# Optimization experiments

Hardware: AMD Instinct MI355X
Metric: run time of the kernel (lower is better)

## Reference

```python
import jax, jax.numpy as jnp
import numpy as np
import math

INPUT_SIZE = 2048
OUTPUT_SIZE = 10000
EPS = 1e-8


def _hadamard_cropped(rows, cols):
    # Sylvester Hadamard: H[i, j] = (-1) ** popcount(i & j), built only on the
    i = np.arange(rows, dtype=np.int64)[:, None]
    j = np.arange(cols, dtype=np.int64)[None, :]
    a = i & j
    nbits = max(rows, cols).bit_length()
    parity = np.zeros((rows, cols), dtype=np.int64)
    for k in range(nbits):
        parity += (a >> k) & 1
    return (1 - 2 * (parity & 1)).astype(np.float32)


def setup_inputs() -> dict:
    key = jax.random.key(0)
    kx, kb = jax.random.split(key)
    init_scale = 1.0 / math.sqrt(OUTPUT_SIZE)
    x = jax.random.normal(kx, (16384, INPUT_SIZE), dtype=jnp.float32)
    proj = jnp.asarray(_hadamard_cropped(OUTPUT_SIZE, INPUT_SIZE))
    scale = jnp.full((1,), init_scale, dtype=jnp.float32)
    bias = jax.random.uniform(kb, (OUTPUT_SIZE,), dtype=jnp.float32,
                              minval=-init_scale, maxval=init_scale)
    return {"x": x, "proj": proj, "scale": scale, "bias": bias}


def reference(x, proj, scale, bias):
    # L2-normalize along last dim (norm + eps, matching torch semantics)
    xn = x / (jnp.linalg.norm(x, axis=-1, keepdims=True) + EPS)
    # linear with cropped Hadamard matrix: [B, in] @ [out, in]^T -> [B, out]
    out = -scale * jnp.einsum('bi,oi->bo', xn, proj)
    return out + bias[None, :]
```

## Files before the change

kernel.cpp:

```cpp
#include <hip/hip_runtime.h>
#include <math.h>


constexpr int N_IN  = 2048;
constexpr int N_OUT = 10000;
constexpr int ROWS_PER_BLOCK = 4;

__global__ __launch_bounds__(256, 5) void fwht_proj_kernel(
    const float* __restrict__ x,
    const float* __restrict__ scale,
    const float* __restrict__ bias,
    float* __restrict__ out)
{
    __shared__ float lds[ROWS_PER_BLOCK * N_IN];

    const int wave = threadIdx.x >> 6;
    const int lane = threadIdx.x & 63;
    const int row  = (blockIdx.x << 2) + wave;

    const float* __restrict__ xrow = x + (size_t)row * N_IN;

    float v[32];
    float ss = 0.0f;
#pragma unroll
    for (int j = 0; j < 32; ++j) {
        v[j] = xrow[j * 64 + lane];
        ss = fmaf(v[j], v[j], ss);
    }
#pragma unroll
    for (int m = 1; m < 64; m <<= 1)
        ss += __shfl_xor(ss, m, 64);
    const float inv = 1.0f / (sqrtf(ss) + 1e-8f);

#pragma unroll
    for (int m = 1; m <= 32; m <<= 1) {
        const bool lo = (lane & m) == 0;
#pragma unroll
        for (int j = 0; j < 32; ++j) {
            float o = __shfl_xor(v[j], m, 64);
            v[j] = lo ? (v[j] + o) : (o - v[j]);
        }
    }
#pragma unroll
    for (int jm = 1; jm <= 16; jm <<= 1) {
#pragma unroll
        for (int j = 0; j < 32; ++j) {
            if ((j & jm) == 0) {
                const float a = v[j], b = v[j ^ jm];
                v[j]      = a + b;
                v[j ^ jm] = a - b;
            }
        }
    }

    float* __restrict__ my = lds + wave * N_IN;
#pragma unroll
    for (int j = 0; j < 32; ++j)
        my[j * 64 + lane] = v[j];

    __syncthreads();

    const float s = -scale[0] * inv;
    float* __restrict__ orow = out + (size_t)row * N_OUT;

    for (int idx = lane; idx < N_OUT / 4; idx += 64) {
        const int o = idx << 2;
        const float4 y  = *reinterpret_cast<const float4*>(my + (o & (N_IN - 1)));
        const float4 bv = *reinterpret_cast<const float4*>(bias + o);
        float4 r;
        r.x = fmaf(s, y.x, bv.x);
        r.y = fmaf(s, y.y, bv.y);
        r.z = fmaf(s, y.z, bv.z);
        r.w = fmaf(s, y.w, bv.w);
        *reinterpret_cast<float4*>(orow + o) = r;
    }
}

extern "C" void kernel_launch(void* const* d_in, const int* in_sizes, int n_in,
                              void* d_out, int out_size, void* d_ws, size_t ws_size,
                              hipStream_t stream) {
    const float* x     = (const float*)d_in[0];
    const float* scale = (const float*)d_in[2];
    const float* bias  = (const float*)d_in[3];
    float* out = (float*)d_out;

    const int rows = in_sizes[0] / N_IN;
    dim3 grid(rows / ROWS_PER_BLOCK), block(256);
    hipLaunchKernelGGL(fwht_proj_kernel, grid, block, 0, stream,
                       x, scale, bias, out);
}
```

Baseline: 165.1 us.

## Keep FWHT result in registers with float4 layout, drop LDS staging

```diff
diff --git a/kernel.cpp b/kernel.cpp
--- a/kernel.cpp
+++ b/kernel.cpp
@@ -1,31 +1,34 @@
 #include <hip/hip_runtime.h>
 #include <math.h>
 
+
+typedef float f32x4 __attribute__((ext_vector_type(4)));
 
 constexpr int N_IN  = 2048;
 constexpr int N_OUT = 10000;
 constexpr int ROWS_PER_BLOCK = 4;
 
-__global__ __launch_bounds__(256, 5) void fwht_proj_kernel(
+__global__ __launch_bounds__(256, 4) void fwht_proj_kernel(
     const float* __restrict__ x,
     const float* __restrict__ scale,
     const float* __restrict__ bias,
     float* __restrict__ out)
 {
-    __shared__ float lds[ROWS_PER_BLOCK * N_IN];
-
     const int wave = threadIdx.x >> 6;
     const int lane = threadIdx.x & 63;
     const int row  = (blockIdx.x << 2) + wave;
 
     const float* __restrict__ xrow = x + (size_t)row * N_IN;
 
-    float v[32];
+    f32x4 v[8];
     float ss = 0.0f;
 #pragma unroll
-    for (int j = 0; j < 32; ++j) {
-        v[j] = xrow[j * 64 + lane];
-        ss = fmaf(v[j], v[j], ss);
+    for (int j = 0; j < 8; ++j) {
+        v[j] = *reinterpret_cast<const f32x4*>(xrow + (j << 8) + (lane << 2));
+        ss = fmaf(v[j].x, v[j].x, ss);
+        ss = fmaf(v[j].y, v[j].y, ss);
+        ss = fmaf(v[j].z, v[j].z, ss);
+        ss = fmaf(v[j].w, v[j].w, ss);
     }
 #pragma unroll
     for (int m = 1; m < 64; m <<= 1)
@@ -33,46 +36,78 @@
     const float inv = 1.0f / (sqrtf(ss) + 1e-8f);
 
 #pragma unroll
+    for (int j = 0; j < 8; ++j) {
+        const f32x4 a = v[j];
+        f32x4 t;
+        t.x = a.x + a.y;  t.y = a.x - a.y;
+        t.z = a.z + a.w;  t.w = a.z - a.w;
+        f32x4 u;
+        u.x = t.x + t.z;  u.y = t.y + t.w;
+        u.z = t.x - t.z;  u.w = t.y - t.w;
+        v[j] = u;
+    }
+#pragma unroll
     for (int m = 1; m <= 32; m <<= 1) {
         const bool lo = (lane & m) == 0;
 #pragma unroll
-        for (int j = 0; j < 32; ++j) {
-            float o = __shfl_xor(v[j], m, 64);
+        for (int j = 0; j < 8; ++j) {
+            f32x4 o;
+            o.x = __shfl_xor(v[j].x, m, 64);
+            o.y = __shfl_xor(v[j].y, m, 64);
+            o.z = __shfl_xor(v[j].z, m, 64);
+            o.w = __shfl_xor(v[j].w, m, 64);
             v[j] = lo ? (v[j] + o) : (o - v[j]);
         }
     }
 #pragma unroll
-    for (int jm = 1; jm <= 16; jm <<= 1) {
+    for (int jm = 1; jm <= 4; jm <<= 1) {
 #pragma unroll
-        for (int j = 0; j < 32; ++j) {
+        for (int j = 0; j < 8; ++j) {
             if ((j & jm) == 0) {
-                const float a = v[j], b = v[j ^ jm];
+                const f32x4 a = v[j], b = v[j ^ jm];
                 v[j]      = a + b;
                 v[j ^ jm] = a - b;
             }
         }
     }
 
-    float* __restrict__ my = lds + wave * N_IN;
-#pragma unroll
-    for (int j = 0; j < 32; ++j)
-        my[j * 64 + lane] = v[j];
-
-    __syncthreads();
-
     const float s = -scale[0] * inv;
     float* __restrict__ orow = out + (size_t)row * N_OUT;
 
-    for (int idx = lane; idx < N_OUT / 4; idx += 64) {
-        const int o = idx << 2;
-        const float4 y  = *reinterpret_cast<const float4*>(my + (o & (N_IN - 1)));
-        const float4 bv = *reinterpret_cast<const float4*>(bias + o);
-        float4 r;
-        r.x = fmaf(s, y.x, bv.x);
-        r.y = fmaf(s, y.y, bv.y);
-        r.z = fmaf(s, y.z, bv.z);
-        r.w = fmaf(s, y.w, bv.w);
-        *reinterpret_cast<float4*>(orow + o) = r;
+#pragma unroll
+    for (int w = 0; w < 4; ++w) {
+#pragma unroll 4
+        for (int j = 0; j < 8; ++j) {
+            const int o = (w << 11) + (j << 8) + (lane << 2);
+            const f32x4 b = *reinterpret_cast<const f32x4*>(bias + o);
+            f32x4 r;
+            r.x = fmaf(s, v[j].x, b.x);
+            r.y = fmaf(s, v[j].y, b.y);
+            r.z = fmaf(s, v[j].z, b.z);
+            r.w = fmaf(s, v[j].w, b.w);
+            *reinterpret_cast<f32x4*>(orow + o) = r;
+        }
+    }
+#pragma unroll 4
+    for (int j = 0; j < 7; ++j) {
+        const int o = 8192 + (j << 8) + (lane << 2);
+        const f32x4 b = *reinterpret_cast<const f32x4*>(bias + o);
+        f32x4 r;
+        r.x = fmaf(s, v[j].x, b.x);
+        r.y = fmaf(s, v[j].y, b.y);
+        r.z = fmaf(s, v[j].z, b.z);
+        r.w = fmaf(s, v[j].w, b.w);
+        *reinterpret_cast<f32x4*>(orow + o) = r;
+    }
+    if (lane < 4) {
+        const int o = 9984 + (lane << 2);
+        const f32x4 b = *reinterpret_cast<const f32x4*>(bias + o);
+        f32x4 r;
+        r.x = fmaf(s, v[7].x, b.x);
+        r.y = fmaf(s, v[7].y, b.y);
+        r.z = fmaf(s, v[7].z, b.z);
+        r.w = fmaf(s, v[7].w, b.w);
+        *reinterpret_cast<f32x4*>(orow + o) = r;
     }
 }
 
```

Measured after the change: 177.4 us. 1.07x slower.
